# Optimization experiments

Hardware: AMD Instinct MI355X
Metric: run time of the kernel (lower is better)

Reference implementation:

```python
import jax, jax.numpy as jnp
import numpy as np

S = 30.0
M_S = 0.1
M_L = 0.4

N = 2048
C = 50257


def setup_inputs() -> dict:
    key = jax.random.key(0)
    k1, k2 = jax.random.split(key)
    score = jax.random.uniform(k1, (N, C), dtype=jnp.float32)
    labels = jax.random.randint(k2, (N,), 0, 2, dtype=jnp.int64)
    return {"score": score, "labels": labels}


def reference(score, labels):
    # margin per sample: m[label], label in {0,1}
    m_table = jnp.array([M_S, M_L], dtype=score.dtype)
    m = m_table[labels]                                   # (N,)
    # target logit per sample (== diagonal(score.T[labels]))
    target = jnp.take_along_axis(score, labels[:, None], axis=1)[:, 0]  # (N,)
    numerator = S * (target - m)                           # (N,)
    # sum over non-target classes of exp(s*score) == full sum - target term
    exp_all = jnp.exp(S * score)                           # (N, C)
    excl_sum = jnp.sum(exp_all, axis=1) - jnp.exp(S * target)
    denominator = jnp.exp(numerator) + excl_sum
    L = numerator - jnp.log(denominator)
    return -jnp.mean(L)
```

## Files before the change

### kernel.cpp

```cpp
#include <hip/hip_runtime.h>
#include <stdint.h>

#define NROWS 2048
#define NCOLS 50257
#define SCALE 30.0f
#define K2 43.28085122666891f

typedef float v4f __attribute__((ext_vector_type(4)));

static __device__ __forceinline__ float fexp2(float x) {
    return __builtin_amdgcn_exp2f(x);
}

__global__ __launch_bounds__(256) void amsoftmax_row_kernel(
    const float* __restrict__ score,
    const int* __restrict__ labels,
    float* __restrict__ partial) {
    const int row = blockIdx.x;
    const int tid = threadIdx.x;
    const float* __restrict__ r = score + (size_t)row * NCOLS;

    const int lab = labels[row];
    const float target = r[lab];
    const float margin = lab ? 0.4f : 0.1f;
    const float num = SCALE * (target - margin);

    const uintptr_t addr = (uintptr_t)r;
    const int mis = (int)(((16u - (addr & 15u)) & 15u) >> 2);

    float a0 = 0.0f, a1 = 0.0f, a2 = 0.0f, a3 = 0.0f;
    for (int j = tid; j < mis; j += 256) a0 += fexp2(K2 * r[j]);

    const int nvec = (NCOLS - mis) >> 2;
    const float* __restrict__ rb = r + mis;

    int j = tid;
    for (; j + 768 < nvec; j += 1024) {
        v4f v0 = *(const v4f*)(rb + 4 * (size_t)j);
        v4f v1 = *(const v4f*)(rb + 4 * (size_t)(j + 256));
        v4f v2 = *(const v4f*)(rb + 4 * (size_t)(j + 512));
        v4f v3 = *(const v4f*)(rb + 4 * (size_t)(j + 768));
        a0 += fexp2(K2 * v0.x) + fexp2(K2 * v0.y) +
              fexp2(K2 * v0.z) + fexp2(K2 * v0.w);
        a1 += fexp2(K2 * v1.x) + fexp2(K2 * v1.y) +
              fexp2(K2 * v1.z) + fexp2(K2 * v1.w);
        a2 += fexp2(K2 * v2.x) + fexp2(K2 * v2.y) +
              fexp2(K2 * v2.z) + fexp2(K2 * v2.w);
        a3 += fexp2(K2 * v3.x) + fexp2(K2 * v3.y) +
              fexp2(K2 * v3.z) + fexp2(K2 * v3.w);
    }
    for (; j < nvec; j += 256) {
        v4f v = *(const v4f*)(rb + 4 * (size_t)j);
        a0 += fexp2(K2 * v.x) + fexp2(K2 * v.y) +
              fexp2(K2 * v.z) + fexp2(K2 * v.w);
    }
    for (int k = mis + (nvec << 2) + tid; k < NCOLS; k += 256) {
        a1 += fexp2(K2 * r[k]);
    }

    float acc = (a0 + a1) + (a2 + a3);
    for (int off = 32; off > 0; off >>= 1) acc += __shfl_down(acc, off);
    __shared__ float wsum[4];
    if ((tid & 63) == 0) wsum[tid >> 6] = acc;
    __syncthreads();
    if (tid == 0) {
        const float total = wsum[0] + wsum[1] + wsum[2] + wsum[3];
        const float excl = total - fexp2(K2 * target);
        const float denom = __expf(num) + excl;
        const float L = num - __logf(denom);
        partial[row] = L;
    }
}

__global__ __launch_bounds__(256) void amsoftmax_reduce_kernel(
    const float* __restrict__ partial,
    float* __restrict__ out) {
    const int tid = threadIdx.x;
    float s = 0.0f;
    #pragma unroll
    for (int i = tid; i < NROWS; i += 256) s += partial[i];
    for (int off = 32; off > 0; off >>= 1) s += __shfl_down(s, off);
    __shared__ float wsum[4];
    if ((tid & 63) == 0) wsum[tid >> 6] = s;
    __syncthreads();
    if (tid == 0) {
        out[0] = -(wsum[0] + wsum[1] + wsum[2] + wsum[3]) *
                 (1.0f / (float)NROWS);
    }
}

extern "C" void kernel_launch(void* const* d_in, const int* in_sizes, int n_in,
                              void* d_out, int out_size, void* d_ws, size_t ws_size,
                              hipStream_t stream) {
    const float* score = (const float*)d_in[0];
    const int* labels = (const int*)d_in[1];
    float* out = (float*)d_out;
    float* partial = (float*)d_ws;

    amsoftmax_row_kernel<<<NROWS, 256, 0, stream>>>(score, labels, partial);
    amsoftmax_reduce_kernel<<<1, 256, 0, stream>>>(partial, out);
}
```

Before: 531.4 us.

## Split each row across two blocks and move target/loss math to finalize

Each row's exp-sum is now computed by two blocks, one per half of the vectorized range, which doubles the grid to 4096 blocks. The per-row target gather and loss computation move into the single-block finalize kernel. The aim is more parallelism and better tail balance across CUs for this memory-bound pass. In exchange the finalize kernel gathers 2048 scattered target values serially in one block, and the workspace holds twice as many partial sums.

```diff
diff --git a/kernel.cpp b/kernel.cpp
--- a/kernel.cpp
+++ b/kernel.cpp
@@ -3,6 +3,7 @@
 
 #define NROWS 2048
 #define NCOLS 50257
+#define HALVES 2
 #define SCALE 30.0f
 #define K2 43.28085122666891f
 
@@ -12,30 +13,33 @@
     return __builtin_amdgcn_exp2f(x);
 }
 
-__global__ __launch_bounds__(256) void amsoftmax_row_kernel(
+__global__ __launch_bounds__(256) void amsoftmax_partial_kernel(
     const float* __restrict__ score,
-    const int* __restrict__ labels,
-    float* __restrict__ partial) {
-    const int row = blockIdx.x;
+    float* __restrict__ psum) {
+    const int row = blockIdx.x >> 1;
+    const int half = blockIdx.x & 1;
     const int tid = threadIdx.x;
     const float* __restrict__ r = score + (size_t)row * NCOLS;
 
-    const int lab = labels[row];
-    const float target = r[lab];
-    const float margin = lab ? 0.4f : 0.1f;
-    const float num = SCALE * (target - margin);
-
     const uintptr_t addr = (uintptr_t)r;
     const int mis = (int)(((16u - (addr & 15u)) & 15u) >> 2);
-
-    float a0 = 0.0f, a1 = 0.0f, a2 = 0.0f, a3 = 0.0f;
-    for (int j = tid; j < mis; j += 256) a0 += fexp2(K2 * r[j]);
-
     const int nvec = (NCOLS - mis) >> 2;
     const float* __restrict__ rb = r + mis;
 
-    int j = tid;
-    for (; j + 768 < nvec; j += 1024) {
+    const int lo = half ? (nvec >> 1) : 0;
+    const int hi = half ? nvec : (nvec >> 1);
+
+    float a0 = 0.0f, a1 = 0.0f, a2 = 0.0f, a3 = 0.0f;
+
+    if (!half) {
+        for (int j = tid; j < mis; j += 256) a0 += fexp2(K2 * r[j]);
+    } else {
+        for (int k = mis + (nvec << 2) + tid; k < NCOLS; k += 256)
+            a1 += fexp2(K2 * r[k]);
+    }
+
+    int j = lo + tid;
+    for (; j + 768 < hi; j += 1024) {
         v4f v0 = *(const v4f*)(rb + 4 * (size_t)j);
         v4f v1 = *(const v4f*)(rb + 4 * (size_t)(j + 256));
         v4f v2 = *(const v4f*)(rb + 4 * (size_t)(j + 512));
@@ -49,13 +53,10 @@
         a3 += fexp2(K2 * v3.x) + fexp2(K2 * v3.y) +
               fexp2(K2 * v3.z) + fexp2(K2 * v3.w);
     }
-    for (; j < nvec; j += 256) {
+    for (; j < hi; j += 256) {
         v4f v = *(const v4f*)(rb + 4 * (size_t)j);
         a0 += fexp2(K2 * v.x) + fexp2(K2 * v.y) +
               fexp2(K2 * v.z) + fexp2(K2 * v.w);
-    }
-    for (int k = mis + (nvec << 2) + tid; k < NCOLS; k += 256) {
-        a1 += fexp2(K2 * r[k]);
     }
 
     float acc = (a0 + a1) + (a2 + a3);
@@ -64,21 +65,28 @@
     if ((tid & 63) == 0) wsum[tid >> 6] = acc;
     __syncthreads();
     if (tid == 0) {
-        const float total = wsum[0] + wsum[1] + wsum[2] + wsum[3];
+        psum[blockIdx.x] = wsum[0] + wsum[1] + wsum[2] + wsum[3];
+    }
+}
+
+__global__ __launch_bounds__(256) void amsoftmax_finalize_kernel(
+    const float* __restrict__ score,
+    const int* __restrict__ labels,
+    const float* __restrict__ psum,
+    float* __restrict__ out) {
+    const int tid = threadIdx.x;
+    float s = 0.0f;
+    for (int row = tid; row < NROWS; row += 256) {
+        const float total = psum[2 * row] + psum[2 * row + 1];
+        const int lab = labels[row];
+        const float target = score[(size_t)row * NCOLS + lab];
+        const float margin = lab ? 0.4f : 0.1f;
+        const float num = SCALE * (target - margin);
         const float excl = total - fexp2(K2 * target);
         const float denom = __expf(num) + excl;
         const float L = num - __logf(denom);
-        partial[row] = L;
+        s += L;
     }
-}
-
-__global__ __launch_bounds__(256) void amsoftmax_reduce_kernel(
-    const float* __restrict__ partial,
-    float* __restrict__ out) {
-    const int tid = threadIdx.x;
-    float s = 0.0f;
-    #pragma unroll
-    for (int i = tid; i < NROWS; i += 256) s += partial[i];
     for (int off = 32; off > 0; off >>= 1) s += __shfl_down(s, off);
     __shared__ float wsum[4];
     if ((tid & 63) == 0) wsum[tid >> 6] = s;
@@ -95,8 +103,8 @@
     const float* score = (const float*)d_in[0];
     const int* labels = (const int*)d_in[1];
     float* out = (float*)d_out;
-    float* partial = (float*)d_ws;
+    float* psum = (float*)d_ws;
 
-    amsoftmax_row_kernel<<<NROWS, 256, 0, stream>>>(score, labels, partial);
-    amsoftmax_reduce_kernel<<<1, 256, 0, stream>>>(partial, out);
+    amsoftmax_partial_kernel<<<NROWS * HALVES, 256, 0, stream>>>(score, psum);
+    amsoftmax_finalize_kernel<<<1, 256, 0, stream>>>(score, labels, psum, out);
 }
```

Result: no change. 532.8 us (+0.3%).
